# Performance work log

Measured on AMD Instinct MI355X. Metric: run time of the kernel, lower is better.

The kernel has to match this reference:

```python
import jax, jax.numpy as jnp
import numpy as np
from jax import lax

V, D, H, HD, L, E, HID, TOPK, B, T = 32000, 1024, 16, 64, 2, 4, 2048, 2, 1, 1024
EPS = 1e-8


def setup_inputs() -> dict:
    key = jax.random.key(0)
    ks = jax.random.split(key, 10)
    s = 0.02
    so = 0.02 / np.sqrt(2 * L)  # o_proj / down_proj init std
    return dict(
        idx=jax.random.randint(ks[0], (B, T), 0, V),
        tok_emb=jax.random.normal(ks[1], (V, D), jnp.float32) * s,
        attn_norm_w=jnp.ones((L, D), jnp.float32),
        q_w=jax.random.normal(ks[2], (L, D, D), jnp.float32) * s,
        q_b=jnp.zeros((L, D), jnp.float32),
        kv_w=jax.random.normal(ks[3], (L, D, 2 * D), jnp.float32) * s,
        kv_b=jnp.zeros((L, 2 * D), jnp.float32),
        o_w=jax.random.normal(ks[4], (L, D, D), jnp.float32) * so,
        o_b=jnp.zeros((L, D), jnp.float32),
        ffn_norm_w=jnp.ones((L, D), jnp.float32),
        router_w=jax.random.normal(ks[5], (L, D, E), jnp.float32) * s,
        gate_w=jax.random.normal(ks[6], (L, E, D, HID), jnp.float32) * s,
        up_w=jax.random.normal(ks[7], (L, E, D, HID), jnp.float32) * s,
        down_w=jax.random.normal(ks[8], (L, E, HID, D), jnp.float32) * so,
        lnf_w=jnp.ones((D,), jnp.float32),
    )


def _rms(x, w):
    return x / jnp.sqrt(jnp.mean(x * x, axis=-1, keepdims=True) + EPS) * w


def reference(idx, tok_emb, attn_norm_w, q_w, q_b, kv_w, kv_b, o_w, o_b,
              ffn_norm_w, router_w, gate_w, up_w, down_w, lnf_w):
    x = tok_emb[idx]  # [B,T,D]

    # ALiBi bias and causal mask (built once; block_size == T here)
    slopes = jnp.arange(1, H + 1, dtype=jnp.float32) / H          # [H]
    pos = jnp.arange(T, dtype=jnp.float32)
    alibi = slopes[:, None, None] * (pos[None, None, :] - pos[None, :, None])  # [H,T,T]
    causal = jnp.arange(T)[None, :] > jnp.arange(T)[:, None]      # True above diagonal

    for l in range(L):
        # --- causal self-attention with ALiBi ---
        h = _rms(x, attn_norm_w[l])
        q = (h @ q_w[l] + q_b[l]).reshape(B, T, H, HD)
        kv = (h @ kv_w[l] + kv_b[l]).reshape(B, T, 2, H, HD)
        k, v = kv[:, :, 0], kv[:, :, 1]
        att = jnp.einsum('bqhd,bkhd->bhqk', q, k) * (1.0 / np.sqrt(HD))
        att = att + alibi[None]
        att = jnp.where(causal, -jnp.inf, att)
        a = jax.nn.softmax(att, axis=-1)
        y = jnp.einsum('bhqk,bkhd->bqhd', a, v).reshape(B, T, D)
        x = x + y @ o_w[l] + o_b[l]

        # --- MoE FFN (top-k routing, SwiGLU experts, depth-scaled down_proj) ---
        hm = _rms(x, ffn_norm_w[l]).reshape(B * T, D)             # [N,D]
        rlog = hm @ router_w[l]                                   # [N,E]
        vals, sel = lax.top_k(rlog, TOPK)                         # [N,K]
        w = jax.nn.softmax(vals.astype(jnp.float32), axis=-1).astype(hm.dtype)
        # dense per-expert compute, combined sparsely via routing weights
        g = jax.nn.silu(jnp.einsum('nd,edh->enh', hm, gate_w[l])) \
            * jnp.einsum('nd,edh->enh', hm, up_w[l])              # [E,N,HID]
        out_e = jnp.einsum('enh,ehd->end', g, down_w[l]) * (1.0 / np.sqrt(l + 1))
        combine = jnp.sum(jax.nn.one_hot(sel, E, dtype=hm.dtype) * w[..., None], axis=1)  # [N,E]
        moe = jnp.einsum('ne,end->nd', combine, out_e).reshape(B, T, D)
        x = x + moe

    logits = _rms(x, lnf_w) @ tok_emb.T  # tied head weight
    return logits
```

## Files before the change

### kernel.cpp

```cpp
#include <hip/hip_runtime.h>
#include <cmath>

typedef __attribute__((ext_vector_type(8))) _Float16 f16x8;
typedef __attribute__((ext_vector_type(8))) unsigned short u16x8;
typedef __attribute__((ext_vector_type(4))) float f32x4;

#define DEV static __device__ __forceinline__

constexpr int Dm   = 1024;
constexpr int HIDm = 2048;
constexpr int NT   = 1024;
constexpr int NV   = 32000;
constexpr float EPSf  = 1e-8f;
constexpr float LOSC  = 4096.0f;
constexpr float ILOSC = 1.0f / 4096.0f;

DEV unsigned short h2u(_Float16 h){ union{_Float16 h; unsigned short u;} v; v.h=h; return v.u; }

DEV f32x4 MF(f16x8 a, f16x8 b, f32x4 c){ return __builtin_amdgcn_mfma_f32_16x16x32_f16(a,b,c,0,0,0); }

typedef __attribute__((address_space(1))) void GV;
typedef __attribute__((address_space(3))) void LV;
DEV void gll16(const void* g, void* l){
  __builtin_amdgcn_global_load_lds((GV*)(__UINTPTR_TYPE__)g, (LV*)l, 16, 0, 0);
}

template<int SPLIT>
DEV void st_sp(unsigned short* __restrict__ hi, unsigned short* __restrict__ lo, size_t o, float v){
  _Float16 hh = (_Float16)v;
  hi[o] = h2u(hh);
  if constexpr (SPLIT==3) lo[o] = h2u((_Float16)((v - (float)hh)*LOSC));
}

__global__ __launch_bounds__(256) void k_gather(
    const int* __restrict__ idx, const float* __restrict__ emb, float* __restrict__ x)
{
  const int t = blockIdx.x;
  const int d = threadIdx.x*4;
  *(float4*)&x[(size_t)t*Dm + d] = *(const float4*)&emb[(size_t)idx[t]*Dm + d];
}

template<int SPLIT>
__global__ __launch_bounds__(256) void k_rms(
    const float* __restrict__ x, const float* __restrict__ w,
    unsigned short* __restrict__ ohi, unsigned short* __restrict__ olo)
{
  const int t = blockIdx.x, tid = threadIdx.x;
  const float* row = x + (size_t)t*Dm;
  float s = 0.f;
  #pragma unroll
  for (int i=0;i<4;++i){ const float v = row[tid + i*256]; s += v*v; }
  #pragma unroll
  for (int d=1; d<64; d<<=1) s += __shfl_xor(s, d);
  __shared__ float red[4];
  if ((tid&63)==0) red[tid>>6] = s;
  __syncthreads();
  const float tot = red[0]+red[1]+red[2]+red[3];
  const float rstd = rsqrtf(tot*(1.0f/Dm) + EPSf);
  #pragma unroll
  for (int i=0;i<4;++i){
    const int c = tid + i*256;
    st_sp<SPLIT>(ohi, olo, (size_t)t*Dm + c, row[c]*rstd*w[c]);
  }
}

__global__ __launch_bounds__(64) void k_router(
    const float* __restrict__ x, const float* __restrict__ nw,
    const float* __restrict__ rw, float* __restrict__ cmb)
{
  const int t = blockIdx.x, lane = threadIdx.x;
  const float* row = x + (size_t)t*Dm;
  float ss = 0.f;
  for (int i=lane; i<Dm; i+=64) ss += row[i]*row[i];
  #pragma unroll
  for (int d=1; d<64; d<<=1) ss += __shfl_xor(ss, d);
  const float rstd = rsqrtf(ss*(1.0f/Dm) + EPSf);
  float lg0=0,lg1=0,lg2=0,lg3=0;
  for (int i=lane; i<Dm; i+=64){
    const float hm = row[i]*rstd*nw[i];
    lg0 += hm*rw[i*4+0]; lg1 += hm*rw[i*4+1];
    lg2 += hm*rw[i*4+2]; lg3 += hm*rw[i*4+3];
  }
  #pragma unroll
  for (int d=1; d<64; d<<=1){
    lg0 += __shfl_xor(lg0,d); lg1 += __shfl_xor(lg1,d);
    lg2 += __shfl_xor(lg2,d); lg3 += __shfl_xor(lg3,d);
  }
  if (lane==0){
    float lg[4] = {lg0,lg1,lg2,lg3};
    int s0 = 0;
    for (int e=1;e<4;++e) if (lg[e] > lg[s0]) s0 = e;
    int s1 = -1;
    for (int e=0;e<4;++e){ if (e==s0) continue; if (s1<0 || lg[e] > lg[s1]) s1 = e; }
    const float eb2 = expf(lg[s1] - lg[s0]);
    const float inv = 1.0f/(1.0f + eb2);
    float o[4] = {0.f,0.f,0.f,0.f};
    o[s0] = inv; o[s1] = eb2*inv;
    cmb[t*4+0]=o[0]; cmb[t*4+1]=o[1]; cmb[t*4+2]=o[2]; cmb[t*4+3]=o[3];
  }
}

template<int SPLIT>
__global__ __launch_bounds__(256) void k_wconv(
    const float* __restrict__ W, unsigned short* __restrict__ Whi,
    unsigned short* __restrict__ Wlo, int K, int N)
{
  __shared__ float tile[64][65];
  const int t = threadIdx.x;
  const int n0 = blockIdx.x*64, k0 = blockIdx.y*64;
  const size_t eb = (size_t)blockIdx.z * (size_t)K * N;
  const int r = t>>2;
  #pragma unroll
  for (int i=0;i<4;++i){
    const int c = (t&3)*16 + i*4;
    *(float4*)&tile[r][c] = *(const float4*)&W[eb + (size_t)(k0+r)*N + n0 + c];
  }
  __syncthreads();
  const int n = t>>2;
  #pragma unroll
  for (int i=0;i<2;++i){
    const int kc = (t&3)*8 + i*32;
    u16x8 hi, lo;
    #pragma unroll
    for (int j=0;j<8;++j){
      const float v = tile[kc+j][n];
      const _Float16 hh = (_Float16)v;
      hi[j] = h2u(hh);
      if constexpr (SPLIT==3) lo[j] = h2u((_Float16)((v-(float)hh)*LOSC));
      else lo[j] = 0;
    }
    *(u16x8*)&Whi[eb + (size_t)(n0+n)*K + k0 + kc] = hi;
    if constexpr (SPLIT==3) *(u16x8*)&Wlo[eb + (size_t)(n0+n)*K + k0 + kc] = lo;
  }
}

template<int SPLIT, int EPI, int ZMODE>
__global__ __launch_bounds__(256) void k_mm(
    const unsigned short* __restrict__ Ahi, const unsigned short* __restrict__ Alo,
    const unsigned short* __restrict__ Bhi, const unsigned short* __restrict__ Blo,
    const float* __restrict__ bias, const float* __restrict__ bias2,
    unsigned short* __restrict__ Ohi, unsigned short* __restrict__ Olo,
    unsigned short* __restrict__ O2hi, unsigned short* __restrict__ O2lo,
    unsigned short* __restrict__ O3hi, unsigned short* __restrict__ O3lo,
    float* __restrict__ part, int lda, int ldb, int K)
{
  constexpr int PL = (SPLIT==3)?2:1;
  __shared__ __align__(16) unsigned short As[PL][128][32];
  __shared__ __align__(16) unsigned short Bs[PL][128][32];
  const int tid=threadIdx.x, wv=tid>>6, lane=tid&63, fr=lane&15, fg=lane>>4;
  const int n0=blockIdx.x*128, r0=blockIdx.y*128, zz=blockIdx.z;
  const int wr=(wv>>1)*64, wc=(wv&1)*64;
  const int sr=lane>>2, sk=(lane&3)*8;

  const f32x4 z4={0.f,0.f,0.f,0.f};
  f32x4 accM[4][4], accC[4][4];
  #pragma unroll
  for (int i=0;i<4;++i)
    #pragma unroll
    for (int j=0;j<4;++j){ accM[i][j]=z4; accC[i][j]=z4; }

  for (int kt=0; kt<K; kt+=32){
    #pragma unroll
    for (int i=0;i<2;++i){
      const int rr = wv*32 + i*16 + sr;
      size_t ao, bo;
      if constexpr (ZMODE==1){
        ao = (size_t)((zz<<10) + r0 + rr)*lda + kt + sk;
        bo = (size_t)zz*((size_t)Dm*HIDm) + (size_t)(n0+rr)*ldb + kt + sk;
      } else if constexpr (ZMODE==2){
        ao = (size_t)(r0+rr)*lda + zz*K + kt + sk;
        bo = (size_t)(n0+rr)*ldb + zz*K + kt + sk;
      } else {
        ao = (size_t)(r0+rr)*lda + kt + sk;
        bo = (size_t)(n0+rr)*ldb + kt + sk;
      }
      gll16(&Ahi[ao], &As[0][wv*32+i*16][0]);
      if constexpr (SPLIT==3) gll16(&Alo[ao], &As[1][wv*32+i*16][0]);
      gll16(&Bhi[bo], &Bs[0][wv*32+i*16][0]);
      if constexpr (SPLIT==3) gll16(&Blo[bo], &Bs[1][wv*32+i*16][0]);
    }
    __syncthreads();
    f16x8 a[4][PL], b[4][PL];
    #pragma unroll
    for (int rt=0;rt<4;++rt)
      #pragma unroll
      for (int p=0;p<PL;++p) a[rt][p] = *(const f16x8*)&As[p][wr+rt*16+fr][fg*8];
    #pragma unroll
    for (int ct=0;ct<4;++ct)
      #pragma unroll
      for (int p=0;p<PL;++p) b[ct][p] = *(const f16x8*)&Bs[p][wc+ct*16+fr][fg*8];
    #pragma unroll
    for (int rt=0;rt<4;++rt)
      #pragma unroll
      for (int ct=0;ct<4;++ct){
        accM[rt][ct] = MF(a[rt][0], b[ct][0], accM[rt][ct]);
        if constexpr (SPLIT==3){
          accC[rt][ct] = MF(a[rt][0], b[ct][1], accC[rt][ct]);
          accC[rt][ct] = MF(a[rt][1], b[ct][0], accC[rt][ct]);
        }
      }
    __syncthreads();
  }

  #pragma unroll
  for (int rt=0;rt<4;++rt)
    #pragma unroll
    for (int ct=0;ct<4;++ct)
      #pragma unroll
      for (int j=0;j<4;++j){
        const int row = r0 + wr + rt*16 + fg*4 + j;
        const int col = n0 + wc + ct*16 + fr;
        float v = accM[rt][ct][j];
        if constexpr (SPLIT==3) v += accC[rt][ct][j]*ILOSC;
        if constexpr (EPI==3){
          if (col < Dm){
            v += bias[col];
            st_sp<SPLIT>(Ohi, Olo, (size_t)row*Dm + col, v);
          } else if (col < 2*Dm){
            v += bias2[col-Dm];
            st_sp<SPLIT>(O2hi, O2lo, (size_t)row*Dm + (col-Dm), v);
          } else {
            v += bias2[col-Dm];
            st_sp<SPLIT>(O3hi, O3lo, (size_t)(col-2*Dm)*NT + row, v);
          }
        } else {
          part[((size_t)zz*NT + row)*Dm + col] = v;
        }
      }
}

template<int SK, bool BIAS>
__global__ __launch_bounds__(256) void k_comb(
    const float* __restrict__ part, const float* __restrict__ bias, float* __restrict__ x)
{
  const int row = blockIdx.x;
  const int c = threadIdx.x*4;
  float4 s = *(float4*)&x[(size_t)row*Dm + c];
  #pragma unroll
  for (int z=0; z<SK; ++z){
    const float4 p = *(const float4*)&part[((size_t)z*NT + row)*Dm + c];
    s.x+=p.x; s.y+=p.y; s.z+=p.z; s.w+=p.w;
  }
  if constexpr (BIAS){
    const float4 b = *(const float4*)&bias[c];
    s.x+=b.x; s.y+=b.y; s.z+=b.z; s.w+=b.w;
  }
  *(float4*)&x[(size_t)row*Dm + c] = s;
}

template<int SPLIT>
__global__ __launch_bounds__(512) void k_guf(
    const unsigned short* __restrict__ Ahi, const unsigned short* __restrict__ Alo,
    const unsigned short* __restrict__ Ghi, const unsigned short* __restrict__ Glo,
    const unsigned short* __restrict__ Uhi, const unsigned short* __restrict__ Ulo,
    const float* __restrict__ cmb,
    unsigned short* __restrict__ Hhi, unsigned short* __restrict__ Hlo, float scale)
{
  constexpr int PL=(SPLIT==3)?2:1;
  __shared__ __align__(16) unsigned short As[PL][128][32];
  __shared__ __align__(16) unsigned short Gs[PL][64][32];
  __shared__ __align__(16) unsigned short Us[PL][64][32];
  const int tid=threadIdx.x, wv=tid>>6, lane=tid&63, fr=lane&15, fg=lane>>4;
  const int n0=blockIdx.x*64, r0=blockIdx.y*128, e=blockIdx.z;
  const int wr=(wv>>1)*32, wc=(wv&1)*32;
  const int sr=lane>>2, sk=(lane&3)*8;
  const size_t ebW = (size_t)e * ((size_t)HIDm*Dm);

  const f32x4 z4={0.f,0.f,0.f,0.f};
  f32x4 aGM[2][2],aGC[2][2],aUM[2][2],aUC[2][2];
  #pragma unroll
  for (int i=0;i<2;++i)
    #pragma unroll
    for (int j=0;j<2;++j){ aGM[i][j]=z4; aGC[i][j]=z4; aUM[i][j]=z4; aUC[i][j]=z4; }

  for (int kt=0; kt<Dm; kt+=32){
    {
      const int rr = wv*16 + sr;
      const size_t ao = (size_t)(r0+rr)*Dm + kt + sk;
      gll16(&Ahi[ao], &As[0][wv*16][0]);
      if constexpr (SPLIT==3) gll16(&Alo[ao], &As[1][wv*16][0]);
    }
    {
      const int rr = (wv&3)*16 + sr;
      const size_t bo = ebW + (size_t)(n0+rr)*Dm + kt + sk;
      if (wv < 4){
        gll16(&Ghi[bo], &Gs[0][(wv&3)*16][0]);
        if constexpr (SPLIT==3) gll16(&Glo[bo], &Gs[1][(wv&3)*16][0]);
      } else {
        gll16(&Uhi[bo], &Us[0][(wv&3)*16][0]);
        if constexpr (SPLIT==3) gll16(&Ulo[bo], &Us[1][(wv&3)*16][0]);
      }
    }
    __syncthreads();
    f16x8 a[2][PL], bg[2][PL], bu[2][PL];
    #pragma unroll
    for (int rt=0;rt<2;++rt)
      #pragma unroll
      for (int p=0;p<PL;++p) a[rt][p] = *(const f16x8*)&As[p][wr+rt*16+fr][fg*8];
    #pragma unroll
    for (int ct=0;ct<2;++ct)
      #pragma unroll
      for (int p=0;p<PL;++p){
        bg[ct][p] = *(const f16x8*)&Gs[p][wc+ct*16+fr][fg*8];
        bu[ct][p] = *(const f16x8*)&Us[p][wc+ct*16+fr][fg*8];
      }
    #pragma unroll
    for (int rt=0;rt<2;++rt)
      #pragma unroll
      for (int ct=0;ct<2;++ct){
        aGM[rt][ct] = MF(a[rt][0], bg[ct][0], aGM[rt][ct]);
        aUM[rt][ct] = MF(a[rt][0], bu[ct][0], aUM[rt][ct]);
        if constexpr (SPLIT==3){
          aGC[rt][ct] = MF(a[rt][0], bg[ct][1], aGC[rt][ct]);
          aGC[rt][ct] = MF(a[rt][1], bg[ct][0], aGC[rt][ct]);
          aUC[rt][ct] = MF(a[rt][0], bu[ct][1], aUC[rt][ct]);
          aUC[rt][ct] = MF(a[rt][1], bu[ct][0], aUC[rt][ct]);
        }
      }
    __syncthreads();
  }
  #pragma unroll
  for (int rt=0;rt<2;++rt)
    #pragma unroll
    for (int ct=0;ct<2;++ct)
      #pragma unroll
      for (int j=0;j<4;++j){
        const int row = r0 + wr + rt*16 + fg*4 + j;
        const int col = n0 + wc + ct*16 + fr;
        float g = aGM[rt][ct][j], u = aUM[rt][ct][j];
        if constexpr (SPLIT==3){ g += aGC[rt][ct][j]*ILOSC; u += aUC[rt][ct][j]*ILOSC; }
        const float cw = cmb[row*4 + e] * scale;
        const float h = (g/(1.0f + expf(-g))) * u * cw;
        st_sp<SPLIT>(Hhi, Hlo, (size_t)((e<<10) + row)*HIDm + col, h);
      }
}

__global__ __launch_bounds__(512) void k_lg(
    const unsigned short* __restrict__ Ahi, const float* __restrict__ emb,
    float* __restrict__ out)
{
  __shared__ __align__(16) unsigned short As[256][32];
  __shared__ __align__(16) unsigned short Bs[128][32];
  const int tid=threadIdx.x, wv=tid>>6, lane=tid&63, fr=lane&15, fg=lane>>4;
  const int n0=blockIdx.x*128, r0=blockIdx.y*256;
  const int wrow=(wv>>2)*128, wcol=(wv&3)*32;
  const int sr=lane>>2, sk=(lane&3)*8;
  const f32x4 z4={0.f,0.f,0.f,0.f};
  f32x4 acc[8][2];
  #pragma unroll
  for (int i=0;i<8;++i){ acc[i][0]=z4; acc[i][1]=z4; }

  for (int kt=0; kt<Dm; kt+=32){
    #pragma unroll
    for (int i=0;i<2;++i){
      const int rr = wv*32 + i*16 + sr;
      gll16(&Ahi[(size_t)(r0+rr)*Dm + kt + sk], &As[wv*32+i*16][0]);
    }
    {
      const int br = tid>>2;
      const int bc = (tid&3)*8;
      const float* s = &emb[(size_t)(n0+br)*Dm + kt + bc];
      const float4 v0 = *(const float4*)s;
      const float4 v1 = *(const float4*)(s+4);
      u16x8 hh;
      hh[0]=h2u((_Float16)v0.x); hh[1]=h2u((_Float16)v0.y);
      hh[2]=h2u((_Float16)v0.z); hh[3]=h2u((_Float16)v0.w);
      hh[4]=h2u((_Float16)v1.x); hh[5]=h2u((_Float16)v1.y);
      hh[6]=h2u((_Float16)v1.z); hh[7]=h2u((_Float16)v1.w);
      *(u16x8*)&Bs[br][bc] = hh;
    }
    __syncthreads();
    f16x8 a[8], b[2];
    #pragma unroll
    for (int rt=0;rt<8;++rt) a[rt] = *(const f16x8*)&As[wrow+rt*16+fr][fg*8];
    #pragma unroll
    for (int ct=0;ct<2;++ct) b[ct] = *(const f16x8*)&Bs[wcol+ct*16+fr][fg*8];
    #pragma unroll
    for (int rt=0;rt<8;++rt)
      #pragma unroll
      for (int ct=0;ct<2;++ct) acc[rt][ct] = MF(a[rt], b[ct], acc[rt][ct]);
    __syncthreads();
  }
  #pragma unroll
  for (int rt=0;rt<8;++rt)
    #pragma unroll
    for (int ct=0;ct<2;++ct)
      #pragma unroll
      for (int j=0;j<4;++j)
        out[(size_t)(r0+wrow+rt*16+fg*4+j)*NV + n0+wcol+ct*16+fr] = acc[rt][ct][j];
}

template<int SPLIT>
__global__ __launch_bounds__(256) void k_attn(
    const unsigned short* __restrict__ qhi, const unsigned short* __restrict__ qlo,
    const unsigned short* __restrict__ khi, const unsigned short* __restrict__ klo,
    const unsigned short* __restrict__ vthi, const unsigned short* __restrict__ vtlo,
    unsigned short* __restrict__ yhi, unsigned short* __restrict__ ylo)
{
  constexpr int PL = (SPLIT==3) ? 2 : 1;
  const int qt = blockIdx.x, hd = blockIdx.y;
  const int tid = threadIdx.x, wv = tid>>6, lane = tid&63;
  const int fr = lane&15, fg = lane>>4;
  const int rbase = qt*64 + wv*16;
  const float slope = (float)(hd+1) * (1.0f/16.0f);

  __shared__ __align__(16) unsigned short Ps[4][PL][16][32];

  f16x8 aq[2][PL];
  #pragma unroll
  for (int c=0;c<2;++c){
    const size_t off = (size_t)(rbase+fr)*Dm + hd*64 + c*32 + fg*8;
    aq[c][0] = *(const f16x8*)&qhi[off];
    if constexpr (SPLIT==3) aq[c][1] = *(const f16x8*)&qlo[off];
  }

  const f32x4 z4 = {0.f,0.f,0.f,0.f};
  f32x4 yM[4], yC[4];
  #pragma unroll
  for (int ct=0;ct<4;++ct){ yM[ct]=z4; yC[ct]=z4; }
  float m[4], lsum[4];
  #pragma unroll
  for (int j=0;j<4;++j){ m[j] = -INFINITY; lsum[j] = 0.f; }

  const int nkt = qt*2 + 2;
  for (int kt=0; kt<nkt; ++kt){
    f32x4 sM[2], sC[2];
    sM[0]=z4; sM[1]=z4; sC[0]=z4; sC[1]=z4;
    #pragma unroll
    for (int kh=0; kh<2; ++kh){
      #pragma unroll
      for (int c=0;c<2;++c){
        const size_t off = (size_t)(kt*32 + kh*16 + fr)*Dm + hd*64 + c*32 + fg*8;
        const f16x8 b0 = *(const f16x8*)&khi[off];
        sM[kh] = MF(aq[c][0], b0, sM[kh]);
        if constexpr (SPLIT==3){
          const f16x8 b1 = *(const f16x8*)&klo[off];
          sC[kh] = MF(aq[c][0], b1, sC[kh]);
          sC[kh] = MF(aq[c][1], b0, sC[kh]);
        }
      }
    }
    float sv[2][4], mx[4];
    #pragma unroll
    for (int j=0;j<4;++j) mx[j] = -INFINITY;
    #pragma unroll
    for (int kh=0; kh<2; ++kh)
      #pragma unroll
      for (int j=0;j<4;++j){
        const int kcol = kt*32 + kh*16 + fr;
        const int row  = rbase + fg*4 + j;
        float s = sM[kh][j];
        if constexpr (SPLIT==3) s += sC[kh][j]*ILOSC;
        s = s*0.125f + slope*(float)(kcol - row);
        sv[kh][j] = (kcol > row) ? -INFINITY : s;
        mx[j] = fmaxf(mx[j], sv[kh][j]);
      }
    #pragma unroll
    for (int d=1; d<16; d<<=1)
      #pragma unroll
      for (int j=0;j<4;++j) mx[j] = fmaxf(mx[j], __shfl_xor(mx[j], d));
    float resc[4];
    #pragma unroll
    for (int j=0;j<4;++j){
      const float mn = fmaxf(m[j], mx[j]);
      resc[j] = expf(m[j] - mn);
      m[j] = mn;
    }
    float p[2][4], psum[4];
    #pragma unroll
    for (int j=0;j<4;++j) psum[j] = 0.f;
    #pragma unroll
    for (int kh=0;kh<2;++kh)
      #pragma unroll
      for (int j=0;j<4;++j){
        const float pv = (sv[kh][j] == -INFINITY) ? 0.f : expf(sv[kh][j] - m[j]);
        p[kh][j] = pv; psum[j] += pv;
      }
    #pragma unroll
    for (int d=1; d<16; d<<=1)
      #pragma unroll
      for (int j=0;j<4;++j) psum[j] += __shfl_xor(psum[j], d);
    #pragma unroll
    for (int j=0;j<4;++j) lsum[j] = lsum[j]*resc[j] + psum[j];
    #pragma unroll
    for (int ct=0;ct<4;++ct)
      #pragma unroll
      for (int j=0;j<4;++j){ yM[ct][j]*=resc[j]; yC[ct][j]*=resc[j]; }
    #pragma unroll
    for (int kh=0;kh<2;++kh)
      #pragma unroll
      for (int j=0;j<4;++j){
        const float pv = p[kh][j];
        _Float16 ph = (_Float16)pv;
        Ps[wv][0][fg*4+j][kh*16+fr] = h2u(ph);
        if constexpr (SPLIT==3)
          Ps[wv][1][fg*4+j][kh*16+fr] = h2u((_Float16)((pv-(float)ph)*LOSC));
      }
    asm volatile("s_waitcnt lgkmcnt(0)" ::: "memory");
    f16x8 pa[PL];
    pa[0] = *(const f16x8*)&Ps[wv][0][fr][fg*8];
    if constexpr (SPLIT==3) pa[1] = *(const f16x8*)&Ps[wv][1][fr][fg*8];
    #pragma unroll
    for (int ct=0;ct<4;++ct){
      const size_t off = (size_t)(hd*64 + ct*16 + fr)*NT + kt*32 + fg*8;
      const f16x8 v0 = *(const f16x8*)&vthi[off];
      yM[ct] = MF(pa[0], v0, yM[ct]);
      if constexpr (SPLIT==3){
        const f16x8 v1 = *(const f16x8*)&vtlo[off];
        yC[ct] = MF(pa[0], v1, yC[ct]);
        yC[ct] = MF(pa[1], v0, yC[ct]);
      }
    }
    asm volatile("s_waitcnt lgkmcnt(0)" ::: "memory");
  }
  #pragma unroll
  for (int ct=0;ct<4;++ct)
    #pragma unroll
    for (int j=0;j<4;++j){
      float v = yM[ct][j];
      if constexpr (SPLIT==3) v += yC[ct][j]*ILOSC;
      v /= lsum[j];
      const size_t off = (size_t)(rbase + fg*4 + j)*Dm + hd*64 + ct*16 + fr;
      st_sp<SPLIT>(yhi, ylo, off, v);
    }
}

struct Ptrs {
  float* x; float* cmb; float* part;
  unsigned short *hhi,*hlo,*qhi,*qlo,*khi,*klo,*vthi,*vtlo,*yhi,*ylo,*Hhi,*Hlo;
  unsigned short *Wqkvh,*Wqkvl,*WOh,*WOl,*WGh,*WGl,*WUh,*WUl,*WDh,*WDl;
};

template<int S>
static void run_layer(const Ptrs& P, int l,
    const float* anw, const float* qw, const float* qb, const float* kvw, const float* kvb,
    const float* ow, const float* ob, const float* fnw, const float* rw,
    const float* gw, const float* uw, const float* dw, float scale, hipStream_t stream)
{
  unsigned short* nul = nullptr;
  k_rms<S><<<dim3(NT), dim3(256), 0, stream>>>(P.x, anw + l*Dm, P.hhi, P.hlo);
  k_wconv<S><<<dim3(16,16,1), dim3(256), 0, stream>>>(qw + (size_t)l*Dm*Dm, P.Wqkvh, P.Wqkvl, Dm, Dm);
  k_wconv<S><<<dim3(32,16,1), dim3(256), 0, stream>>>(kvw + (size_t)l*Dm*2*Dm,
      P.Wqkvh + (size_t)Dm*Dm, P.Wqkvl + (size_t)Dm*Dm, Dm, 2*Dm);
  k_wconv<S><<<dim3(16,16,1), dim3(256), 0, stream>>>(ow + (size_t)l*Dm*Dm, P.WOh, P.WOl, Dm, Dm);
  k_mm<S,3,0><<<dim3(24,8), dim3(256), 0, stream>>>(P.hhi, P.hlo, P.Wqkvh, P.Wqkvl,
      qb + l*Dm, kvb + l*2*Dm, P.qhi, P.qlo, P.khi, P.klo, P.vthi, P.vtlo,
      nullptr, Dm, Dm, Dm);
  k_attn<S><<<dim3(16,16), dim3(256), 0, stream>>>(P.qhi,P.qlo,P.khi,P.klo,P.vthi,P.vtlo,P.yhi,P.ylo);
  k_mm<S,4,2><<<dim3(8,8,4), dim3(256), 0, stream>>>(P.yhi, P.ylo, P.WOh, P.WOl,
      nullptr, nullptr, nul, nul, nul, nul, nul, nul, P.part, Dm, Dm, 256);
  k_comb<4,true><<<dim3(NT), dim3(256), 0, stream>>>(P.part, ob + l*Dm, P.x);
  k_router<<<dim3(NT), dim3(64), 0, stream>>>(P.x, fnw + l*Dm, rw + (size_t)l*Dm*4, P.cmb);
  k_rms<S><<<dim3(NT), dim3(256), 0, stream>>>(P.x, fnw + l*Dm, P.hhi, P.hlo);
  k_wconv<S><<<dim3(32,16,4), dim3(256), 0, stream>>>(gw + (size_t)l*4*Dm*HIDm, P.WGh, P.WGl, Dm, HIDm);
  k_wconv<S><<<dim3(32,16,4), dim3(256), 0, stream>>>(uw + (size_t)l*4*Dm*HIDm, P.WUh, P.WUl, Dm, HIDm);
  k_guf<S><<<dim3(32,8,4), dim3(512), 0, stream>>>(P.hhi, P.hlo, P.WGh, P.WGl, P.WUh, P.WUl,
      P.cmb, P.Hhi, P.Hlo, scale);
  k_wconv<S><<<dim3(16,32,4), dim3(256), 0, stream>>>(dw + (size_t)l*4*HIDm*Dm, P.WDh, P.WDl, HIDm, Dm);
  k_mm<S,4,1><<<dim3(8,8,4), dim3(256), 0, stream>>>(P.Hhi, P.Hlo, P.WDh, P.WDl,
      nullptr, nullptr, nul, nul, nul, nul, nul, nul, P.part, HIDm, HIDm, HIDm);
  k_comb<4,false><<<dim3(NT), dim3(256), 0, stream>>>(P.part, nullptr, P.x);
}

extern "C" void kernel_launch(void* const* d_in, const int* in_sizes, int n_in,
                              void* d_out, int out_size, void* d_ws, size_t ws_size,
                              hipStream_t stream)
{
  (void)in_sizes; (void)n_in; (void)out_size; (void)ws_size;
  const int*   idx = (const int*)d_in[0];
  const float* emb = (const float*)d_in[1];
  const float* anw = (const float*)d_in[2];
  const float* qw  = (const float*)d_in[3];
  const float* qb  = (const float*)d_in[4];
  const float* kvw = (const float*)d_in[5];
  const float* kvb = (const float*)d_in[6];
  const float* ow  = (const float*)d_in[7];
  const float* ob  = (const float*)d_in[8];
  const float* fnw = (const float*)d_in[9];
  const float* rw  = (const float*)d_in[10];
  const float* gw  = (const float*)d_in[11];
  const float* uw  = (const float*)d_in[12];
  const float* dw  = (const float*)d_in[13];
  const float* lnf = (const float*)d_in[14];

  constexpr size_t MB = (size_t)1<<20;
  char* sc = (char*)d_out;
  Ptrs P;
  P.x     = (float*)sc;
  P.hhi   = (unsigned short*)(sc + 4*MB);
  P.hlo   = (unsigned short*)(sc + 6*MB);
  P.qhi   = (unsigned short*)(sc + 8*MB);
  P.qlo   = (unsigned short*)(sc + 10*MB);
  P.khi   = (unsigned short*)(sc + 12*MB);
  P.klo   = (unsigned short*)(sc + 14*MB);
  P.vthi  = (unsigned short*)(sc + 16*MB);
  P.vtlo  = (unsigned short*)(sc + 18*MB);
  P.yhi   = (unsigned short*)(sc + 20*MB);
  P.ylo   = (unsigned short*)(sc + 22*MB);
  P.cmb   = (float*)(sc + 24*MB);
  P.Hhi   = (unsigned short*)(sc + 25*MB);
  P.Hlo   = (unsigned short*)(sc + 41*MB);
  P.Wqkvh = (unsigned short*)(sc + 57*MB);
  P.Wqkvl = (unsigned short*)(sc + 63*MB);
  P.WOh   = (unsigned short*)(sc + 69*MB);
  P.WOl   = (unsigned short*)(sc + 71*MB);
  P.WGh   = (unsigned short*)(sc + 57*MB);
  P.WGl   = (unsigned short*)(sc + 73*MB);
  P.WUh   = (unsigned short*)(sc + 89*MB);
  P.WUl   = (unsigned short*)(sc + 105*MB);
  P.WDh   = (unsigned short*)(sc + 57*MB);
  P.WDl   = (unsigned short*)(sc + 73*MB);
  P.part  = (float*)(sc + 89*MB);
  unsigned short* xhat = (unsigned short*)d_ws;
  float* out = (float*)d_out;

  k_gather<<<dim3(NT), dim3(256), 0, stream>>>(idx, emb, P.x);

  run_layer<3>(P, 0, anw, qw, qb, kvw, kvb, ow, ob, fnw, rw, gw, uw, dw, 1.0f, stream);
  run_layer<1>(P, 1, anw, qw, qb, kvw, kvb, ow, ob, fnw, rw, gw, uw, dw, 0.70710678f, stream);

  k_rms<1><<<dim3(NT), dim3(256), 0, stream>>>(P.x, lnf, xhat, nullptr);
  k_lg<<<dim3(250,4), dim3(512), 0, stream>>>(xhat, emb, out);
}
```

Before: 898.6 us.

## Enlarge per-warp tiles in gate-up and logits kernels for more reuse

The fused gate/up MoE kernel now runs 256 threads instead of 512, and each wave computes a 64x32 tile, so every B fragment is reused across four row tiles. The logits GEMM widens its block tile to 256x256 with 64-column warp tiles. The 2D grid becomes a 1D grid with the row-block index as the fast-varying dimension, so the four row blocks sharing an embedding tile run close together. This cuts LDS reads and repeated fp32-to-fp16 conversion of the embedding per MFMA. The cost is higher register pressure from larger accumulator arrays, which may lower occupancy, and fewer blocks per launch.

```diff
diff --git a/kernel.cpp b/kernel.cpp
--- a/kernel.cpp
+++ b/kernel.cpp
@@ -249,7 +249,7 @@
 }
 
 template<int SPLIT>
-__global__ __launch_bounds__(512) void k_guf(
+__global__ __launch_bounds__(256) void k_guf(
     const unsigned short* __restrict__ Ahi, const unsigned short* __restrict__ Alo,
     const unsigned short* __restrict__ Ghi, const unsigned short* __restrict__ Glo,
     const unsigned short* __restrict__ Uhi, const unsigned short* __restrict__ Ulo,
@@ -262,39 +262,39 @@
   __shared__ __align__(16) unsigned short Us[PL][64][32];
   const int tid=threadIdx.x, wv=tid>>6, lane=tid&63, fr=lane&15, fg=lane>>4;
   const int n0=blockIdx.x*64, r0=blockIdx.y*128, e=blockIdx.z;
-  const int wr=(wv>>1)*32, wc=(wv&1)*32;
+  const int wr=(wv>>1)*64, wc=(wv&1)*32;
   const int sr=lane>>2, sk=(lane&3)*8;
   const size_t ebW = (size_t)e * ((size_t)HIDm*Dm);
 
   const f32x4 z4={0.f,0.f,0.f,0.f};
-  f32x4 aGM[2][2],aGC[2][2],aUM[2][2],aUC[2][2];
-  #pragma unroll
-  for (int i=0;i<2;++i)
+  f32x4 aGM[4][2],aGC[4][2],aUM[4][2],aUC[4][2];
+  #pragma unroll
+  for (int i=0;i<4;++i)
     #pragma unroll
     for (int j=0;j<2;++j){ aGM[i][j]=z4; aGC[i][j]=z4; aUM[i][j]=z4; aUC[i][j]=z4; }
 
   for (int kt=0; kt<Dm; kt+=32){
+    #pragma unroll
+    for (int i=0;i<2;++i){
+      const int rr = wv*32 + i*16 + sr;
+      const size_t ao = (size_t)(r0+rr)*Dm + kt + sk;
+      gll16(&Ahi[ao], &As[0][wv*32+i*16][0]);
+      if constexpr (SPLIT==3) gll16(&Alo[ao], &As[1][wv*32+i*16][0]);
+    }
     {
       const int rr = wv*16 + sr;
-      const size_t ao = (size_t)(r0+rr)*Dm + kt + sk;
-      gll16(&Ahi[ao], &As[0][wv*16][0]);
-      if constexpr (SPLIT==3) gll16(&Alo[ao], &As[1][wv*16][0]);
-    }
-    {
-      const int rr = (wv&3)*16 + sr;
       const size_t bo = ebW + (size_t)(n0+rr)*Dm + kt + sk;
-      if (wv < 4){
-        gll16(&Ghi[bo], &Gs[0][(wv&3)*16][0]);
-        if constexpr (SPLIT==3) gll16(&Glo[bo], &Gs[1][(wv&3)*16][0]);
-      } else {
-        gll16(&Uhi[bo], &Us[0][(wv&3)*16][0]);
-        if constexpr (SPLIT==3) gll16(&Ulo[bo], &Us[1][(wv&3)*16][0]);
+      gll16(&Ghi[bo], &Gs[0][wv*16][0]);
+      gll16(&Uhi[bo], &Us[0][wv*16][0]);
+      if constexpr (SPLIT==3){
+        gll16(&Glo[bo], &Gs[1][wv*16][0]);
+        gll16(&Ulo[bo], &Us[1][wv*16][0]);
       }
     }
     __syncthreads();
-    f16x8 a[2][PL], bg[2][PL], bu[2][PL];
-    #pragma unroll
-    for (int rt=0;rt<2;++rt)
+    f16x8 a[4][PL], bg[2][PL], bu[2][PL];
+    #pragma unroll
+    for (int rt=0;rt<4;++rt)
       #pragma unroll
       for (int p=0;p<PL;++p) a[rt][p] = *(const f16x8*)&As[p][wr+rt*16+fr][fg*8];
     #pragma unroll
@@ -305,7 +305,7 @@
         bu[ct][p] = *(const f16x8*)&Us[p][wc+ct*16+fr][fg*8];
       }
     #pragma unroll
-    for (int rt=0;rt<2;++rt)
+    for (int rt=0;rt<4;++rt)
       #pragma unroll
       for (int ct=0;ct<2;++ct){
         aGM[rt][ct] = MF(a[rt][0], bg[ct][0], aGM[rt][ct]);
@@ -320,7 +320,7 @@
     __syncthreads();
   }
   #pragma unroll
-  for (int rt=0;rt<2;++rt)
+  for (int rt=0;rt<4;++rt)
     #pragma unroll
     for (int ct=0;ct<2;++ct)
       #pragma unroll
@@ -340,15 +340,18 @@
     float* __restrict__ out)
 {
   __shared__ __align__(16) unsigned short As[256][32];
-  __shared__ __align__(16) unsigned short Bs[128][32];
+  __shared__ __align__(16) unsigned short Bs[256][32];
   const int tid=threadIdx.x, wv=tid>>6, lane=tid&63, fr=lane&15, fg=lane>>4;
-  const int n0=blockIdx.x*128, r0=blockIdx.y*256;
-  const int wrow=(wv>>2)*128, wcol=(wv&3)*32;
+  const int bid = blockIdx.x;
+  const int n0 = (bid>>2)*256, r0 = (bid&3)*256;
+  const int wrow=(wv>>2)*128, wcol=(wv&3)*64;
   const int sr=lane>>2, sk=(lane&3)*8;
   const f32x4 z4={0.f,0.f,0.f,0.f};
-  f32x4 acc[8][2];
-  #pragma unroll
-  for (int i=0;i<8;++i){ acc[i][0]=z4; acc[i][1]=z4; }
+  f32x4 acc[8][4];
+  #pragma unroll
+  for (int i=0;i<8;++i)
+    #pragma unroll
+    for (int j=0;j<4;++j) acc[i][j]=z4;
 
   for (int kt=0; kt<Dm; kt+=32){
     #pragma unroll
@@ -356,8 +359,9 @@
       const int rr = wv*32 + i*16 + sr;
       gll16(&Ahi[(size_t)(r0+rr)*Dm + kt + sk], &As[wv*32+i*16][0]);
     }
-    {
-      const int br = tid>>2;
+    #pragma unroll
+    for (int i=0;i<2;++i){
+      const int br = i*128 + (tid>>2);
       const int bc = (tid&3)*8;
       const float* s = &emb[(size_t)(n0+br)*Dm + kt + bc];
       const float4 v0 = *(const float4*)s;
@@ -370,21 +374,21 @@
       *(u16x8*)&Bs[br][bc] = hh;
     }
     __syncthreads();
-    f16x8 a[8], b[2];
+    f16x8 a[8], b[4];
     #pragma unroll
     for (int rt=0;rt<8;++rt) a[rt] = *(const f16x8*)&As[wrow+rt*16+fr][fg*8];
     #pragma unroll
-    for (int ct=0;ct<2;++ct) b[ct] = *(const f16x8*)&Bs[wcol+ct*16+fr][fg*8];
+    for (int ct=0;ct<4;++ct) b[ct] = *(const f16x8*)&Bs[wcol+ct*16+fr][fg*8];
     #pragma unroll
     for (int rt=0;rt<8;++rt)
       #pragma unroll
-      for (int ct=0;ct<2;++ct) acc[rt][ct] = MF(a[rt], b[ct], acc[rt][ct]);
+      for (int ct=0;ct<4;++ct) acc[rt][ct] = MF(a[rt], b[ct], acc[rt][ct]);
     __syncthreads();
   }
   #pragma unroll
   for (int rt=0;rt<8;++rt)
     #pragma unroll
-    for (int ct=0;ct<2;++ct)
+    for (int ct=0;ct<4;++ct)
       #pragma unroll
       for (int j=0;j<4;++j)
         out[(size_t)(r0+wrow+rt*16+fg*4+j)*NV + n0+wcol+ct*16+fr] = acc[rt][ct][j];
@@ -554,7 +558,7 @@
   k_rms<S><<<dim3(NT), dim3(256), 0, stream>>>(P.x, fnw + l*Dm, P.hhi, P.hlo);
   k_wconv<S><<<dim3(32,16,4), dim3(256), 0, stream>>>(gw + (size_t)l*4*Dm*HIDm, P.WGh, P.WGl, Dm, HIDm);
   k_wconv<S><<<dim3(32,16,4), dim3(256), 0, stream>>>(uw + (size_t)l*4*Dm*HIDm, P.WUh, P.WUl, Dm, HIDm);
-  k_guf<S><<<dim3(32,8,4), dim3(512), 0, stream>>>(P.hhi, P.hlo, P.WGh, P.WGl, P.WUh, P.WUl,
+  k_guf<S><<<dim3(32,8,4), dim3(256), 0, stream>>>(P.hhi, P.hlo, P.WGh, P.WGl, P.WUh, P.WUl,
       P.cmb, P.Hhi, P.Hlo, scale);
   k_wconv<S><<<dim3(16,32,4), dim3(256), 0, stream>>>(dw + (size_t)l*4*HIDm*Dm, P.WDh, P.WDl, HIDm, Dm);
   k_mm<S,4,1><<<dim3(8,8,4), dim3(256), 0, stream>>>(P.Hhi, P.Hlo, P.WDh, P.WDl,
@@ -620,5 +624,5 @@
   run_layer<1>(P, 1, anw, qw, qb, kvw, kvb, ow, ob, fnw, rw, gw, uw, dw, 0.70710678f, stream);
 
   k_rms<1><<<dim3(NT), dim3(256), 0, stream>>>(P.x, lnf, xhat, nullptr);
-  k_lg<<<dim3(250,4), dim3(512), 0, stream>>>(xhat, emb, out);
-}
+  k_lg<<<dim3(500), dim3(512), 0, stream>>>(xhat, emb, out);
+}
```

Result: slower. 1.003 ms (+11.6%).
